# Kernel tuning notes

Measured on AMD Instinct MI355X. Metric: run time of the kernel, lower is better.

## Reference

```python
import jax, jax.numpy as jnp
import numpy as np

NUM_NODES = 39   # nodes per graph (hardcoded in module)
K = 10           # kNN neighbors (hardcoded)
HID = 256
NUM_CLASSES = 2
B = 512          # number of graphs
EPS = 1e-5


def _edge_conv(xg, W, b):
    """DynamicEdgeConv with max aggregation.
    xg: [B, N, F]. Builds kNN graph per-graph (Euclidean), edge feature
    [x_i, x_j - x_i], MLP(ReLU), max over neighbors. Self is its own
    nearest neighbor (matches torch_cluster.knn with x==y).
    """
    bsz, n, f = xg.shape
    sq = jnp.sum(xg * xg, axis=-1)                      # [B, N]
    d = sq[:, :, None] + sq[:, None, :] - 2.0 * jnp.einsum('bnf,bmf->bnm', xg, xg)
    _, idx = jax.lax.top_k(-d, K)                       # [B, N, K] smallest distances
    xj = xg[jnp.arange(bsz)[:, None, None], idx]        # [B, N, K, F]
    xi = xg[:, :, None, :]                              # [B, N, 1, F]
    e = jnp.concatenate([jnp.broadcast_to(xi, xj.shape), xj - xi], axis=-1)  # [B,N,K,2F]
    h = jax.nn.relu(jnp.einsum('bnkc,ch->bnkh', e, W) + b)
    return jnp.max(h, axis=2)                           # [B, N, H]


def _bn(h, gamma, beta):
    # BatchNorm1d over all nodes (training-mode batch stats, biased var)
    mean = jnp.mean(h, axis=(0, 1), keepdims=True)
    var = jnp.var(h, axis=(0, 1), keepdims=True)
    return (h - mean) * jax.lax.rsqrt(var + EPS) * gamma + beta


def setup_inputs() -> dict:
    key = jax.random.key(0)
    ks = jax.random.split(key, 12)
    f_in = NUM_NODES
    x = jax.random.normal(ks[0], (B * NUM_NODES, f_in), dtype=jnp.float32)
    batch = jnp.repeat(jnp.arange(B, dtype=jnp.int32), NUM_NODES)
    def lin(k, fin, fout):
        s = 1.0 / np.sqrt(fin)
        k1, k2 = jax.random.split(k)
        W = jax.random.uniform(k1, (fin, fout), jnp.float32, -s, s)
        b = jax.random.uniform(k2, (fout,), jnp.float32, -s, s)
        return W, b
    W1, b1 = lin(ks[1], 2 * f_in, HID)
    W2, b2 = lin(ks[2], 2 * HID, HID)
    W3, b3 = lin(ks[3], 2 * HID, HID)
    Wl, bl = lin(ks[4], HID, NUM_CLASSES)
    g1 = jnp.ones((HID,), jnp.float32); be1 = jnp.zeros((HID,), jnp.float32)
    g2 = jnp.ones((HID,), jnp.float32); be2 = jnp.zeros((HID,), jnp.float32)
    g3 = jnp.ones((HID,), jnp.float32); be3 = jnp.zeros((HID,), jnp.float32)
    return dict(x=x, batch=batch, W1=W1, b1=b1, W2=W2, b2=b2, W3=W3, b3=b3,
                g1=g1, be1=be1, g2=g2, be2=be2, g3=g3, be3=be3, Wl=Wl, bl=bl)


def reference(x, batch, W1, b1, W2, b2, W3, b3, g1, be1, g2, be2, g3, be3, Wl, bl):
    # Graphs are contiguous with fixed NUM_NODES nodes each (batch == repeat(arange(B))),
    # so reshape implements per-graph kNN and global_mean_pool exactly.
    bsz = x.shape[0] // NUM_NODES
    xg = x.reshape(bsz, NUM_NODES, -1)
    h = _edge_conv(xg, W1, b1)
    h = jax.nn.relu(_bn(h, g1, be1))
    h = _edge_conv(h, W2, b2)
    h = jax.nn.relu(_bn(h, g2, be2))
    h = _edge_conv(h, W3, b3)
    h = _bn(h, g3, be3)
    pooled = jnp.mean(h, axis=1)                        # global_mean_pool -> [B, H]
    logits = pooled @ Wl + bl
    return jax.nn.softmax(logits, axis=1)
```

## Files before the change

### kernel.cpp

```cpp
#include <hip/hip_runtime.h>
#include <hip/hip_bf16.h>
#include <stdint.h>

#define NG 512
#define NN 39
#define FIN0 39
#define HID 256
#define KNN 10
#define NROWS (NG * NN)
#define BNEPS 1e-5f

typedef __hip_bfloat16 bf16;
typedef __attribute__((ext_vector_type(8))) short s16x8;
typedef __attribute__((ext_vector_type(4))) float f32x4;

__device__ __forceinline__ void split_bf16(float v, bf16& hi, bf16& lo) {
  hi = __float2bfloat16(v);
  lo = __float2bfloat16(v - __bfloat162float(hi));
}

__device__ __forceinline__ void ld_b128(s16x8& d, const bf16* base, unsigned voff) {
  asm volatile("global_load_dwordx4 %0, %1, %2"
               : "=v"(d) : "v"(voff), "s"(base));
}
#define WAITV4 do { asm volatile("s_waitcnt vmcnt(4)"); __builtin_amdgcn_sched_barrier(0); } while (0)
#define WAITV0 do { asm volatile("s_waitcnt vmcnt(0)"); __builtin_amdgcn_sched_barrier(0); } while (0)

__device__ __forceinline__ float wfold(const float* __restrict__ W, int F, int c, int k) {
  if (k >= F) return 0.f;
  return (c < HID) ? (W[k * HID + c] - W[(F + k) * HID + c])
                   : W[(F + k) * HID + (c - HID)];
}

__global__ void k_prepw(const float* __restrict__ W1, const float* __restrict__ W2,
                        const float* __restrict__ W3,
                        bf16* __restrict__ W1Th, bf16* __restrict__ W1Tl,
                        bf16* __restrict__ W2Th, bf16* __restrict__ W2Tl,
                        bf16* __restrict__ W3Th, bf16* __restrict__ W3Tl) {
  int d = (blockIdx.x * 256 + threadIdx.x) * 4;
  const float* W; bf16 *Th, *Tl; int nks, F;
  if (d < 512 * 64) { W = W1; Th = W1Th; Tl = W1Tl; nks = 2; F = FIN0; }
  else {
    d -= 512 * 64;
    if (d < 512 * 256) { W = W2; Th = W2Th; Tl = W2Tl; nks = 8; F = HID; }
    else {
      d -= 512 * 256;
      if (d < 512 * 256) { W = W3; Th = W3Th; Tl = W3Tl; nks = 8; F = HID; }
      else return;
    }
  }
  const int frag = d >> 9, wi = d & 511, li = wi >> 3, e0 = wi & 7;
  const int fr = li & 15, fq = li >> 4;
  const int ks = frag % nks, cb = frag / nks;
  const int c = (cb >> 2) * 64 + 4 * fr + (cb & 3);
  const int k0 = ks * 32 + fq * 8 + e0;
  union U { bf16 b[4]; uint64_t u; } h, l;
#pragma unroll
  for (int t = 0; t < 4; t++) split_bf16(wfold(W, F, c, k0 + t), h.b[t], l.b[t]);
  *(uint64_t*)(Th + d) = h.u;
  *(uint64_t*)(Tl + d) = l.u;
}

#define VSTR 260
#define RSTR 260
template <int K, bool FIRST>
__global__ __launch_bounds__(512, 4) void k_fused(const float* __restrict__ fin,
                                                  const float* __restrict__ st,
                                                  const bf16* __restrict__ BTh,
                                                  const bf16* __restrict__ BTl,
                                                  const float* __restrict__ bias,
                                                  float* __restrict__ h_out,
                                                  float* __restrict__ part) {
  constexpr int XBYTES = 48 * K * 2 * 2;
  constexpr int ALIAS = (NN * VSTR + 8 * RSTR) * 4;
  constexpr int SBASE = (XBYTES > ALIAS) ? XBYTES : ((ALIAS + 15) & ~15);
  __shared__ __align__(16) char smem[SBASE + 6240 + 160 + 1568];
  bf16* Xh = (bf16*)smem;
  bf16* Xl = Xh + 48 * K;
  float* vsh = (float*)smem;
  float* red = (float*)(smem + NN * VSTR * 4);
  float* dmat = (float*)(smem + SBASE);
  float* sqv  = (float*)(smem + SBASE + 6240);
  int*   idxs = (int*)(smem + SBASE + 6240 + 160);

  const int b = blockIdx.x, tid = threadIdx.x;
  const int wv = tid >> 6, ln = tid & 63;
  const int fr = ln & 15, fq = ln >> 4;
  const size_t base = (size_t)b * NN;

  constexpr int G4 = K / 4;
  for (int t = tid; t < 48 * G4; t += 512) {
    const int row = t / G4, g4 = t % G4;
    union { bf16 b4[4]; uint64_t u; } ph, pl;
    if (row < NN) {
      float v[4];
      if (FIRST) {
#pragma unroll
        for (int j = 0; j < 4; j++) {
          const int k = g4 * 4 + j;
          v[j] = (k < FIN0) ? fin[(base + row) * FIN0 + k] : 0.f;
        }
      } else {
        const f32x4 hv = *(const f32x4*)&fin[(base + row) * HID + g4 * 4];
#pragma unroll
        for (int j = 0; j < 4; j++) {
          const int c = g4 * 4 + j;
          v[j] = fmaxf(hv[j] * st[c] + st[HID + c], 0.f);
        }
      }
#pragma unroll
      for (int j = 0; j < 4; j++) split_bf16(v[j], ph.b4[j], pl.b4[j]);
    } else { ph.u = 0; pl.u = 0; }
    const int addr = row * K + ((((g4 >> 1) ^ (row & 7)) << 3)) + ((g4 & 1) * 4);
    *(uint64_t*)&Xh[addr] = ph.u;
    *(uint64_t*)&Xl[addr] = pl.u;
  }
  __syncthreads();

  for (int p = wv; p < 9; p += 8) {
    const int mi = p / 3, ni = p % 3;
    f32x4 acg = (f32x4){0.f, 0.f, 0.f, 0.f};
    const int ar = mi * 16 + fr, br = ni * 16 + fr;
#pragma unroll
    for (int ks = 0; ks < K / 32; ks++) {
      const int ga = ((ks * 4 + fq) ^ (ar & 7)) << 3;
      const int gb = ((ks * 4 + fq) ^ (br & 7)) << 3;
      const s16x8 avh = *(const s16x8*)&Xh[ar * K + ga];
      const s16x8 avl = *(const s16x8*)&Xl[ar * K + ga];
      const s16x8 bvh = *(const s16x8*)&Xh[br * K + gb];
      const s16x8 bvl = *(const s16x8*)&Xl[br * K + gb];
      acg = __builtin_amdgcn_mfma_f32_16x16x32_bf16(avh, bvh, acg, 0, 0, 0);
      acg = __builtin_amdgcn_mfma_f32_16x16x32_bf16(avh, bvl, acg, 0, 0, 0);
      acg = __builtin_amdgcn_mfma_f32_16x16x32_bf16(avl, bvh, acg, 0, 0, 0);
    }
    const int oc = ni * 16 + fr;
    if (oc < NN) {
#pragma unroll
      for (int r = 0; r < 4; r++) {
        const int orow = mi * 16 + fq * 4 + r;
        if (orow < NN) dmat[orow * 40 + oc] = acg[r];
      }
    }
  }
  __syncthreads();

  if (tid < NN) sqv[tid] = dmat[tid * 40 + tid];
  __syncthreads();
  for (int t = tid; t < NN * NN; t += 512) {
    const int i = t / NN, j = t - i * NN;
    dmat[i * 40 + j] = sqv[i] + sqv[j] - 2.f * dmat[i * 40 + j];
  }
  __syncthreads();

  const int grp = tid >> 2, l4 = tid & 3;
  if (grp < NN) {
    float dv[10];
#pragma unroll
    for (int s = 0; s < 10; s++) {
      const int j = l4 + s * 4;
      dv[s] = (j < NN) ? dmat[grp * 40 + j] : 3.4e38f;
    }
    unsigned taken = 0;
    for (int k = 0; k < KNN; k++) {
      float bv = 3.4e38f;
      int bi = 1 << 30;
#pragma unroll
      for (int s = 0; s < 10; s++) {
        const float v = ((taken >> s) & 1u) ? 3.4e38f : dv[s];
        const int j = l4 + s * 4;
        if (v < bv || (v == bv && j < bi)) { bv = v; bi = j; }
      }
#pragma unroll
      for (int m = 1; m < 4; m <<= 1) {
        const float ov = __shfl_xor(bv, m, 64);
        const int oi = __shfl_xor(bi, m, 64);
        if (ov < bv || (ov == bv && oi < bi)) { bv = ov; bi = oi; }
      }
      if ((bi & 3) == l4) taken |= 1u << (bi >> 2);
      if (l4 == 0) idxs[grp * 10 + k] = bi;
    }
  }

  constexpr int NKS = K / 32;
  f32x4 acc[3][4];
#pragma unroll
  for (int m = 0; m < 3; m++)
#pragma unroll
    for (int n = 0; n < 4; n++) acc[m][n] = (f32x4){0.f, 0.f, 0.f, 0.f};

  unsigned fb[4];
#pragma unroll
  for (int n = 0; n < 4; n++)
    fb[n] = ((unsigned)((wv * 4 + n) * NKS) << 10) + (unsigned)(ln * 16);

  s16x8 bufH[4], bufL[4];
#pragma unroll
  for (int n = 0; n < 4; n++) ld_b128(bufH[n], BTh, fb[n]);

#pragma unroll
  for (int ks = 0; ks < NKS; ks++) {
#pragma unroll
    for (int n = 0; n < 4; n++) ld_b128(bufL[n], BTl, fb[n] + (unsigned)ks * 1024);
    WAITV4;
#pragma unroll
    for (int m = 0; m < 3; m++) {
      const int row = m * 16 + fr;
      const int g = ((ks * 4 + fq) ^ (row & 7)) << 3;
      const s16x8 ah = *(const s16x8*)&Xh[row * K + g];
      const s16x8 al = *(const s16x8*)&Xl[row * K + g];
#pragma unroll
      for (int n = 0; n < 4; n++) {
        acc[m][n] = __builtin_amdgcn_mfma_f32_16x16x32_bf16(ah, bufH[n], acc[m][n], 0, 0, 0);
        acc[m][n] = __builtin_amdgcn_mfma_f32_16x16x32_bf16(al, bufH[n], acc[m][n], 0, 0, 0);
      }
    }
    if (ks + 1 < NKS) {
#pragma unroll
      for (int n = 0; n < 4; n++) ld_b128(bufH[n], BTh, fb[n] + (unsigned)(ks + 1) * 1024);
      WAITV4;
    } else {
      WAITV0;
    }
#pragma unroll
    for (int m = 0; m < 3; m++) {
      const int row = m * 16 + fr;
      const int g = ((ks * 4 + fq) ^ (row & 7)) << 3;
      const s16x8 ah = *(const s16x8*)&Xh[row * K + g];
#pragma unroll
      for (int n = 0; n < 4; n++)
        acc[m][n] = __builtin_amdgcn_mfma_f32_16x16x32_bf16(ah, bufL[n], acc[m][n], 0, 0, 0);
    }
  }
  __syncthreads();

  if (wv >= 4) {
    const int c0 = (wv - 4) * 64 + fr * 4;
#pragma unroll
    for (int m = 0; m < 3; m++)
#pragma unroll
      for (int r = 0; r < 4; r++) {
        const int row = m * 16 + fq * 4 + r;
        if (row < NN) {
          const f32x4 v4 = (f32x4){acc[m][0][r], acc[m][1][r], acc[m][2][r], acc[m][3][r]};
          *(f32x4*)&vsh[row * VSTR + c0] = v4;
        }
      }
  } else {
    const int c0 = wv * 64 + fr * 4;
    const f32x4 bv = *(const f32x4*)&bias[c0];
#pragma unroll
    for (int n = 0; n < 4; n++)
#pragma unroll
      for (int m = 0; m < 3; m++)
#pragma unroll
        for (int r = 0; r < 4; r++) acc[m][n][r] += bv[n];
  }
  __syncthreads();

  if (wv < 4) {
    const int c0 = wv * 64 + fr * 4;
    f32x4 s1 = (f32x4){0.f, 0.f, 0.f, 0.f}, s2 = (f32x4){0.f, 0.f, 0.f, 0.f};
#pragma unroll
    for (int m = 0; m < 3; m++)
#pragma unroll
      for (int r = 0; r < 4; r++) {
        const int row = m * 16 + fq * 4 + r;
        if (row < NN) {
          int nb[10];
#pragma unroll
          for (int k = 0; k < KNN; k++) nb[k] = idxs[row * 10 + k];
          f32x4 vm = (f32x4){-3.4e38f, -3.4e38f, -3.4e38f, -3.4e38f};
#pragma unroll
          for (int k = 0; k < KNN; k++) {
            const f32x4 t4 = *(const f32x4*)&vsh[nb[k] * VSTR + c0];
            vm[0] = fmaxf(vm[0], t4[0]); vm[1] = fmaxf(vm[1], t4[1]);
            vm[2] = fmaxf(vm[2], t4[2]); vm[3] = fmaxf(vm[3], t4[3]);
          }
          f32x4 h4;
#pragma unroll
          for (int j = 0; j < 4; j++) h4[j] = fmaxf(acc[m][j][r] + vm[j], 0.f);
          *(f32x4*)&h_out[(size_t)(base + row) * HID + c0] = h4;
#pragma unroll
          for (int j = 0; j < 4; j++) { s1[j] += h4[j]; s2[j] += h4[j] * h4[j]; }
        }
      }
    *(f32x4*)&red[fq * RSTR + c0] = s1;
    *(f32x4*)&red[(4 + fq) * RSTR + c0] = s2;
  }
  __syncthreads();
  if (tid < HID) {
    part[(size_t)b * 512 + tid] =
        red[0 * RSTR + tid] + red[1 * RSTR + tid] + red[2 * RSTR + tid] + red[3 * RSTR + tid];
    part[(size_t)b * 512 + HID + tid] =
        red[4 * RSTR + tid] + red[5 * RSTR + tid] + red[6 * RSTR + tid] + red[7 * RSTR + tid];
  }
}

__global__ __launch_bounds__(256) void k_stats(const float* __restrict__ part,
                                               const float* __restrict__ gam,
                                               const float* __restrict__ bet,
                                               float* __restrict__ st) {
  __shared__ float rs[4], rq[4];
  const int c = blockIdx.x, tid = threadIdx.x;
  float s = part[(size_t)tid * 512 + c] + part[(size_t)(tid + 256) * 512 + c];
  float q = part[(size_t)tid * 512 + HID + c] + part[(size_t)(tid + 256) * 512 + HID + c];
#pragma unroll
  for (int m = 32; m >= 1; m >>= 1) { s += __shfl_down(s, m, 64); q += __shfl_down(q, m, 64); }
  if ((tid & 63) == 0) { rs[tid >> 6] = s; rq[tid >> 6] = q; }
  __syncthreads();
  if (tid == 0) {
    s = rs[0] + rs[1] + rs[2] + rs[3];
    q = rq[0] + rq[1] + rq[2] + rq[3];
    const float mean = s * (1.f / NROWS);
    const float var = q * (1.f / NROWS) - mean * mean;
    const float sc = gam[c] * rsqrtf(var + BNEPS);
    st[c] = sc;
    st[HID + c] = bet[c] - mean * sc;
  }
}

__global__ __launch_bounds__(256) void k_final(const float* __restrict__ h3,
                                               const float* __restrict__ st,
                                               const float* __restrict__ Wl,
                                               const float* __restrict__ bl,
                                               float* __restrict__ out) {
  __shared__ float r0[HID], r1[HID];
  const int b = blockIdx.x, c = threadIdx.x;
  float s = 0.f;
  for (int n = 0; n < NN; n++) s += h3[((size_t)b * NN + n) * HID + c];
  const float pooled = (s * (1.f / NN)) * st[c] + st[HID + c];
  r0[c] = pooled * Wl[c * 2 + 0];
  r1[c] = pooled * Wl[c * 2 + 1];
  __syncthreads();
  for (int stp = 128; stp > 0; stp >>= 1) {
    if (c < stp) { r0[c] += r0[c + stp]; r1[c] += r1[c + stp]; }
    __syncthreads();
  }
  if (c == 0) {
    const float l0 = r0[0] + bl[0], l1 = r1[0] + bl[1];
    const float mx = fmaxf(l0, l1);
    const float e0 = expf(l0 - mx), e1 = expf(l1 - mx);
    const float inv = 1.f / (e0 + e1);
    out[b * 2 + 0] = e0 * inv;
    out[b * 2 + 1] = e1 * inv;
  }
}

extern "C" void kernel_launch(void* const* d_in, const int* in_sizes, int n_in,
                              void* d_out, int out_size, void* d_ws, size_t ws_size,
                              hipStream_t stream) {
  const float* x   = (const float*)d_in[0];
  const float* W1  = (const float*)d_in[2];
  const float* b1  = (const float*)d_in[3];
  const float* W2  = (const float*)d_in[4];
  const float* b2  = (const float*)d_in[5];
  const float* W3  = (const float*)d_in[6];
  const float* b3  = (const float*)d_in[7];
  const float* g1  = (const float*)d_in[8];
  const float* be1 = (const float*)d_in[9];
  const float* g2  = (const float*)d_in[10];
  const float* be2 = (const float*)d_in[11];
  const float* g3  = (const float*)d_in[12];
  const float* be3 = (const float*)d_in[13];
  const float* Wl  = (const float*)d_in[14];
  const float* bl  = (const float*)d_in[15];

  char* ws = (char*)d_ws;
  size_t off = 0;
  auto alloc = [&](size_t bytes) {
    size_t o = off;
    off += (bytes + 255) & ~(size_t)255;
    return o;
  };
  bf16* W1Th = (bf16*)(ws + alloc(512 * 64 * 2));
  bf16* W1Tl = (bf16*)(ws + alloc(512 * 64 * 2));
  bf16* W2Th = (bf16*)(ws + alloc(512 * 256 * 2));
  bf16* W2Tl = (bf16*)(ws + alloc(512 * 256 * 2));
  bf16* W3Th = (bf16*)(ws + alloc(512 * 256 * 2));
  bf16* W3Tl = (bf16*)(ws + alloc(512 * 256 * 2));
  float* hA  = (float*)(ws + alloc((size_t)NROWS * HID * 4));
  float* hB  = (float*)(ws + alloc((size_t)NROWS * HID * 4));
  float* part = (float*)(ws + alloc((size_t)NG * 512 * 4));
  float* st1 = (float*)(ws + alloc(512 * 4));
  float* st2 = (float*)(ws + alloc(512 * 4));
  float* st3 = (float*)(ws + alloc(512 * 4));
  if (off > ws_size) return;

  k_prepw<<<288, 256, 0, stream>>>(W1, W2, W3, W1Th, W1Tl, W2Th, W2Tl, W3Th, W3Tl);

  k_fused<64, true><<<NG, 512, 0, stream>>>(x, nullptr, W1Th, W1Tl, b1, hA, part);
  k_stats<<<HID, 256, 0, stream>>>(part, g1, be1, st1);

  k_fused<256, false><<<NG, 512, 0, stream>>>(hA, st1, W2Th, W2Tl, b2, hB, part);
  k_stats<<<HID, 256, 0, stream>>>(part, g2, be2, st2);

  k_fused<256, false><<<NG, 512, 0, stream>>>(hB, st2, W3Th, W3Tl, b3, hA, part);
  k_stats<<<HID, 256, 0, stream>>>(part, g3, be3, st3);

  k_final<<<NG, 256, 0, stream>>>(hA, st3, Wl, bl, (float*)d_out);
}
```

Baseline: 100.4 us.

## Issue input loads up front and prefetch weight tiles before kNN in edge conv

The input staging is rewritten so that for later layers each thread issues all of its global loads for three rows together, with 8-wide vectors, and then applies BN+ReLU and the bf16 split. The first bf16 weight-fragment loads are moved ahead of the distance/kNN phase so their latency overlaps that work. The X fragments for each k-step are loaded once into registers before the MFMA loops instead of inside them. The final pooling loop is partially unrolled. This raises register pressure, since the weight buffers stay live across the kNN phase.

```diff
diff --git a/kernel.cpp b/kernel.cpp
--- a/kernel.cpp
+++ b/kernel.cpp
@@ -20,8 +20,10 @@
 }
 
 __device__ __forceinline__ void ld_b128(s16x8& d, const bf16* base, unsigned voff) {
-  asm volatile("global_load_dwordx4 %0, %1, %2"
-               : "=v"(d) : "v"(voff), "s"(base));
+  asm volatile("global_load_dwordx4 %0, %1, %2" : "=v"(d) : "v"(voff), "s"(base));
+}
+__device__ __forceinline__ void ld_f32x4(f32x4& d, const float* base, unsigned voff) {
+  asm volatile("global_load_dwordx4 %0, %1, %2" : "=v"(d) : "v"(voff), "s"(base));
 }
 #define WAITV4 do { asm volatile("s_waitcnt vmcnt(4)"); __builtin_amdgcn_sched_barrier(0); } while (0)
 #define WAITV0 do { asm volatile("s_waitcnt vmcnt(0)"); __builtin_amdgcn_sched_barrier(0); } while (0)
@@ -87,34 +89,77 @@
   const int wv = tid >> 6, ln = tid & 63;
   const int fr = ln & 15, fq = ln >> 4;
   const size_t base = (size_t)b * NN;
-
-  constexpr int G4 = K / 4;
-  for (int t = tid; t < 48 * G4; t += 512) {
-    const int row = t / G4, g4 = t % G4;
-    union { bf16 b4[4]; uint64_t u; } ph, pl;
-    if (row < NN) {
-      float v[4];
-      if (FIRST) {
-#pragma unroll
-        for (int j = 0; j < 4; j++) {
-          const int k = g4 * 4 + j;
-          v[j] = (k < FIN0) ? fin[(base + row) * FIN0 + k] : 0.f;
+  constexpr int NKS = K / 32;
+
+  if (FIRST) {
+    if (tid < 48 * 8) {
+      const int row = tid >> 3, g = tid & 7;
+      union { bf16 b8[8]; s16x8 v; } ph, pl;
+      if (row < NN) {
+#pragma unroll
+        for (int j = 0; j < 8; j++) {
+          const int k = g * 8 + j;
+          const float x = (k < FIN0) ? fin[(base + row) * FIN0 + k] : 0.f;
+          split_bf16(x, ph.b8[j], pl.b8[j]);
         }
       } else {
-        const f32x4 hv = *(const f32x4*)&fin[(base + row) * HID + g4 * 4];
-#pragma unroll
-        for (int j = 0; j < 4; j++) {
-          const int c = g4 * 4 + j;
-          v[j] = fmaxf(hv[j] * st[c] + st[HID + c], 0.f);
-        }
-      }
-#pragma unroll
-      for (int j = 0; j < 4; j++) split_bf16(v[j], ph.b4[j], pl.b4[j]);
-    } else { ph.u = 0; pl.u = 0; }
-    const int addr = row * K + ((((g4 >> 1) ^ (row & 7)) << 3)) + ((g4 & 1) * 4);
-    *(uint64_t*)&Xh[addr] = ph.u;
-    *(uint64_t*)&Xl[addr] = pl.u;
-  }
+#pragma unroll
+        for (int j = 0; j < 8; j++) { ph.b8[j] = __float2bfloat16(0.f); pl.b8[j] = ph.b8[j]; }
+      }
+      const int ad = row * K + ((g ^ (row & 7)) << 3);
+      *(s16x8*)&Xh[ad] = ph.v;
+      *(s16x8*)&Xl[ad] = pl.v;
+    }
+  } else {
+    const int r0 = tid >> 5, g = tid & 31;
+    const unsigned o0 = (unsigned)((((base + r0) * HID) + g * 8) * 4);
+    const unsigned rstep = (unsigned)(16 * HID * 4);
+    f32x4 a0, a1, b0, b1, c0v, c1v;
+    ld_f32x4(a0, fin, o0);             ld_f32x4(a1, fin, o0 + 16);
+    ld_f32x4(b0, fin, o0 + rstep);     ld_f32x4(b1, fin, o0 + rstep + 16);
+    ld_f32x4(c0v, fin, o0 + 2 * rstep); ld_f32x4(c1v, fin, o0 + 2 * rstep + 16);
+    const f32x4 sc0 = *(const f32x4*)&st[g * 8];
+    const f32x4 sc1 = *(const f32x4*)&st[g * 8 + 4];
+    const f32x4 sh0 = *(const f32x4*)&st[HID + g * 8];
+    const f32x4 sh1 = *(const f32x4*)&st[HID + g * 8 + 4];
+    WAITV0;
+    auto proc = [&](int row, const f32x4& lo4, const f32x4& hi4) {
+      union { bf16 b8[8]; s16x8 v; } ph, pl;
+#pragma unroll
+      for (int j = 0; j < 4; j++) {
+        const float v = fmaxf(lo4[j] * sc0[j] + sh0[j], 0.f);
+        split_bf16(v, ph.b8[j], pl.b8[j]);
+      }
+#pragma unroll
+      for (int j = 0; j < 4; j++) {
+        const float v = fmaxf(hi4[j] * sc1[j] + sh1[j], 0.f);
+        split_bf16(v, ph.b8[4 + j], pl.b8[4 + j]);
+      }
+      const int ad = row * K + ((g ^ (row & 7)) << 3);
+      *(s16x8*)&Xh[ad] = ph.v;
+      *(s16x8*)&Xl[ad] = pl.v;
+    };
+    proc(r0, a0, a1);
+    proc(r0 + 16, b0, b1);
+    const int r2 = r0 + 32;
+    if (r2 < NN) proc(r2, c0v, c1v);
+    else {
+      union { bf16 b8[8]; s16x8 v; } z;
+#pragma unroll
+      for (int j = 0; j < 8; j++) z.b8[j] = __float2bfloat16(0.f);
+      const int ad = r2 * K + ((g ^ (r2 & 7)) << 3);
+      *(s16x8*)&Xh[ad] = z.v;
+      *(s16x8*)&Xl[ad] = z.v;
+    }
+  }
+
+  unsigned fb[4];
+#pragma unroll
+  for (int n = 0; n < 4; n++)
+    fb[n] = ((unsigned)((wv * 4 + n) * NKS) << 10) + (unsigned)(ln * 16);
+  s16x8 bufH[4], bufL[4];
+#pragma unroll
+  for (int n = 0; n < 4; n++) ld_b128(bufH[n], BTh, fb[n]);
   __syncthreads();
 
   for (int p = wv; p < 9; p += 8) {
@@ -122,7 +167,7 @@
     f32x4 acg = (f32x4){0.f, 0.f, 0.f, 0.f};
     const int ar = mi * 16 + fr, br = ni * 16 + fr;
 #pragma unroll
-    for (int ks = 0; ks < K / 32; ks++) {
+    for (int ks = 0; ks < NKS; ks++) {
       const int ga = ((ks * 4 + fq) ^ (ar & 7)) << 3;
       const int gb = ((ks * 4 + fq) ^ (br & 7)) << 3;
       const s16x8 avh = *(const s16x8*)&Xh[ar * K + ga];
@@ -181,38 +226,35 @@
     }
   }
 
-  constexpr int NKS = K / 32;
   f32x4 acc[3][4];
 #pragma unroll
   for (int m = 0; m < 3; m++)
 #pragma unroll
     for (int n = 0; n < 4; n++) acc[m][n] = (f32x4){0.f, 0.f, 0.f, 0.f};
 
-  unsigned fb[4];
-#pragma unroll
-  for (int n = 0; n < 4; n++)
-    fb[n] = ((unsigned)((wv * 4 + n) * NKS) << 10) + (unsigned)(ln * 16);
-
-  s16x8 bufH[4], bufL[4];
-#pragma unroll
-  for (int n = 0; n < 4; n++) ld_b128(bufH[n], BTh, fb[n]);
-
 #pragma unroll
   for (int ks = 0; ks < NKS; ks++) {
 #pragma unroll
     for (int n = 0; n < 4; n++) ld_b128(bufL[n], BTl, fb[n] + (unsigned)ks * 1024);
+    s16x8 ah0, ah1, ah2, al0, al1, al2;
+    {
+      const int r0w = fr, r1w = 16 + fr, r2w = 32 + fr;
+      const int g0 = ((ks * 4 + fq) ^ (r0w & 7)) << 3;
+      const int g1 = ((ks * 4 + fq) ^ (r1w & 7)) << 3;
+      const int g2 = ((ks * 4 + fq) ^ (r2w & 7)) << 3;
+      ah0 = *(const s16x8*)&Xh[r0w * K + g0]; al0 = *(const s16x8*)&Xl[r0w * K + g0];
+      ah1 = *(const s16x8*)&Xh[r1w * K + g1]; al1 = *(const s16x8*)&Xl[r1w * K + g1];
+      ah2 = *(const s16x8*)&Xh[r2w * K + g2]; al2 = *(const s16x8*)&Xl[r2w * K + g2];
+    }
     WAITV4;
 #pragma unroll
-    for (int m = 0; m < 3; m++) {
-      const int row = m * 16 + fr;
-      const int g = ((ks * 4 + fq) ^ (row & 7)) << 3;
-      const s16x8 ah = *(const s16x8*)&Xh[row * K + g];
-      const s16x8 al = *(const s16x8*)&Xl[row * K + g];
-#pragma unroll
-      for (int n = 0; n < 4; n++) {
-        acc[m][n] = __builtin_amdgcn_mfma_f32_16x16x32_bf16(ah, bufH[n], acc[m][n], 0, 0, 0);
-        acc[m][n] = __builtin_amdgcn_mfma_f32_16x16x32_bf16(al, bufH[n], acc[m][n], 0, 0, 0);
-      }
+    for (int n = 0; n < 4; n++) {
+      acc[0][n] = __builtin_amdgcn_mfma_f32_16x16x32_bf16(ah0, bufH[n], acc[0][n], 0, 0, 0);
+      acc[0][n] = __builtin_amdgcn_mfma_f32_16x16x32_bf16(al0, bufH[n], acc[0][n], 0, 0, 0);
+      acc[1][n] = __builtin_amdgcn_mfma_f32_16x16x32_bf16(ah1, bufH[n], acc[1][n], 0, 0, 0);
+      acc[1][n] = __builtin_amdgcn_mfma_f32_16x16x32_bf16(al1, bufH[n], acc[1][n], 0, 0, 0);
+      acc[2][n] = __builtin_amdgcn_mfma_f32_16x16x32_bf16(ah2, bufH[n], acc[2][n], 0, 0, 0);
+      acc[2][n] = __builtin_amdgcn_mfma_f32_16x16x32_bf16(al2, bufH[n], acc[2][n], 0, 0, 0);
     }
     if (ks + 1 < NKS) {
 #pragma unroll
@@ -222,13 +264,10 @@
       WAITV0;
     }
 #pragma unroll
-    for (int m = 0; m < 3; m++) {
-      const int row = m * 16 + fr;
-      const int g = ((ks * 4 + fq) ^ (row & 7)) << 3;
-      const s16x8 ah = *(const s16x8*)&Xh[row * K + g];
-#pragma unroll
-      for (int n = 0; n < 4; n++)
-        acc[m][n] = __builtin_amdgcn_mfma_f32_16x16x32_bf16(ah, bufL[n], acc[m][n], 0, 0, 0);
+    for (int n = 0; n < 4; n++) {
+      acc[0][n] = __builtin_amdgcn_mfma_f32_16x16x32_bf16(ah0, bufL[n], acc[0][n], 0, 0, 0);
+      acc[1][n] = __builtin_amdgcn_mfma_f32_16x16x32_bf16(ah1, bufL[n], acc[1][n], 0, 0, 0);
+      acc[2][n] = __builtin_amdgcn_mfma_f32_16x16x32_bf16(ah2, bufL[n], acc[2][n], 0, 0, 0);
     }
   }
   __syncthreads();
@@ -327,6 +366,7 @@
   __shared__ float r0[HID], r1[HID];
   const int b = blockIdx.x, c = threadIdx.x;
   float s = 0.f;
+#pragma unroll 13
   for (int n = 0; n < NN; n++) s += h3[((size_t)b * NN + n) * HID + c];
   const float pooled = (s * (1.f / NN)) * st[c] + st[HID + c];
   r0[c] = pooled * Wl[c * 2 + 0];
```

After: 99.56 us, median of 2. No clear change (-0.8%).
